# Optimization experiments

Hardware: AMD Instinct MI355X
Metric: run time of the kernel (lower is better)

## Reference

```python
import jax, jax.numpy as jnp
import numpy as np

K = 5000  # module's self.dim

def setup_inputs() -> dict:
    key = jax.random.key(0)
    x = jax.random.normal(key, (50_000_000,), dtype=jnp.float32)
    return {"x": x}

def reference(x):
    # top-k values and their indices (lax.top_k returns them sorted by value,
    # but the subsequent argsort over indices restores original-index order,
    # matching torch.topk(sorted=False) + argsort + gather exactly)
    vals, idx = jax.lax.top_k(x, K)          # [K], [K]
    order = jnp.argsort(idx)                 # permutation restoring input order
    return vals[order]                       # [K] order-preserving top-k subset
```

## Files before the change

### kernel.cpp

```cpp
#include <hip/hip_runtime.h>

#define K_TOP 5000
#define NBIN 2048
#define NB_BUCKET 4096
#define TILE4 2048
#define TARGET_SAMPLED 94u

__device__ __forceinline__ unsigned f2key(float f) {
    unsigned u = __float_as_uint(f);
    return (u & 0x80000000u) ? ~u : (u | 0x80000000u);
}
__device__ __forceinline__ float key2f(unsigned k) {
    unsigned u = (k & 0x80000000u) ? (k ^ 0x80000000u) : ~k;
    return __uint_as_float(u);
}

__global__ __launch_bounds__(256) void k_sample(const float4* __restrict__ x4, long n4,
                                                unsigned* __restrict__ hist) {
    __shared__ unsigned lh[NBIN];
    for (int i = threadIdx.x; i < NBIN; i += 256) lh[i] = 0;
    __syncthreads();
    int wave = threadIdx.x >> 6;
    int lane = threadIdx.x & 63;
    long gw = (long)blockIdx.x * 4 + wave;
    long totW = (long)gridDim.x * 4;
    long nChunk = (n4 + 8191) / 8192;
    for (long c = gw; c < nChunk; c += totW) {
        long i = c * 8192 + lane;
        if (i < n4) {
            float4 v = x4[i];
            atomicAdd(&lh[f2key(v.x) >> 21], 1u);
            atomicAdd(&lh[f2key(v.y) >> 21], 1u);
            atomicAdd(&lh[f2key(v.z) >> 21], 1u);
            atomicAdd(&lh[f2key(v.w) >> 21], 1u);
        }
    }
    __syncthreads();
    for (int i = threadIdx.x; i < NBIN; i += 256) {
        unsigned c = lh[i];
        if (c) atomicAdd(&hist[i], c);
    }
}

__global__ __launch_bounds__(256) void k_findbin(const unsigned* __restrict__ hist,
                                                 unsigned* __restrict__ ctrl) {
    __shared__ unsigned lh[NBIN];
    __shared__ unsigned gs[64];
    for (int i = threadIdx.x; i < NBIN; i += 256) lh[i] = hist[i];
    __syncthreads();
    int t = threadIdx.x;
    if (t < 64) {
        unsigned s = 0;
        for (int j = 0; j < 32; j++) s += lh[t * 32 + j];
        gs[t] = s;
    }
    __syncthreads();
    if (t == 0) {
        unsigned cum = 0;
        int g = 63;
        for (; g > 0; g--) { if (cum + gs[g] >= TARGET_SAMPLED) break; cum += gs[g]; }
        int b = g * 32 + 31;
        for (; b > g * 32; b--) { if (cum + lh[b] >= TARGET_SAMPLED) break; cum += lh[b]; }
        ctrl[1] = ((unsigned)b) << 21;
    }
}

__global__ __launch_bounds__(256) void k_compact(const float4* __restrict__ x4, long n4,
                                                 long n, const float* __restrict__ x,
                                                 unsigned* __restrict__ ctrl,
                                                 unsigned* __restrict__ candKey,
                                                 unsigned* __restrict__ candIdx,
                                                 unsigned capC) {
    unsigned L = ctrl[1];
    float Lf = key2f(L);
    long base = (long)blockIdx.x * TILE4 + threadIdx.x;
    float4 v[8];
#pragma unroll
    for (int j = 0; j < 8; j++) {
        long i = base + (long)j * 256;
        v[j] = make_float4(-1e38f, -1e38f, -1e38f, -1e38f);
        if (i < n4) v[j] = x4[i];
    }
    float m = -1e38f;
#pragma unroll
    for (int j = 0; j < 8; j++)
        m = fmaxf(m, fmaxf(fmaxf(v[j].x, v[j].y), fmaxf(v[j].z, v[j].w)));
    if (__any(m >= Lf)) {
#pragma unroll
        for (int j = 0; j < 8; j++) {
            long i = base + (long)j * 256;
            if (i < n4) {
                unsigned bb = (unsigned)(i * 4);
                const float* pv = (const float*)&v[j];
#pragma unroll
                for (int c = 0; c < 4; c++) {
                    float f = pv[c];
                    if (f >= Lf) {
                        unsigned p = atomicAdd(&ctrl[0], 1u);
                        if (p < capC) { candKey[p] = f2key(f); candIdx[p] = bb + (unsigned)c; }
                    }
                }
            }
        }
    }
    if (blockIdx.x == 0 && threadIdx.x < (int)(n & 3)) {
        float f = x[n4 * 4 + threadIdx.x];
        if (f >= Lf) {
            unsigned p = atomicAdd(&ctrl[0], 1u);
            if (p < capC) { candKey[p] = f2key(f); candIdx[p] = (unsigned)(n4 * 4 + threadIdx.x); }
        }
    }
}

__global__ __launch_bounds__(1024) void k_final(const unsigned* __restrict__ candKey,
                                                const unsigned* __restrict__ candIdx,
                                                unsigned* __restrict__ ctrl, unsigned capC,
                                                unsigned* __restrict__ selKey,
                                                unsigned* __restrict__ selIdx,
                                                unsigned* __restrict__ selKeyS,
                                                unsigned* __restrict__ selIdxS,
                                                float* __restrict__ out, long n, int bshift) {
    __shared__ unsigned h[NB_BUCKET * 2];
    __shared__ unsigned part[1024];
    __shared__ unsigned part2[32];
    __shared__ unsigned res[2];
    __shared__ unsigned sScalar;
    const int t = threadIdx.x;
    unsigned Nc = ctrl[0]; if (Nc > capC) Nc = capC;
    unsigned L = ctrl[1];

    unsigned mk = 0;
    for (unsigned i = t; i < Nc; i += 1024) { unsigned k = candKey[i]; if (k > mk) mk = k; }
    part[t] = mk;
    __syncthreads();
    if (t < 32) { unsigned m = 0; for (int j = 0; j < 32; j++) { unsigned v = part[t * 32 + j]; if (v > m) m = v; } part2[t] = m; }
    __syncthreads();
    if (t == 0) { unsigned m = 0; for (int j = 0; j < 32; j++) if (part2[j] > m) m = part2[j]; sScalar = m; }
    __syncthreads();
    unsigned maxK = sScalar;

    unsigned lo = L, target = K_TOP;
    unsigned range = maxK - lo;
    int shift = 0;
    while ((range >> shift) >= NBIN) shift++;
    for (;;) {
        int nb = (int)(range >> shift) + 1;
        for (int i = t; i < nb; i += 1024) h[i] = 0;
        __syncthreads();
        for (unsigned i = t; i < Nc; i += 1024) {
            unsigned d = candKey[i] - lo;
            if (d <= range) atomicAdd(&h[d >> shift], 1u);
        }
        __syncthreads();
        int ng = (nb + 31) >> 5;
        if (t < ng) {
            unsigned s = 0; int b0 = t * 32, e = b0 + 32; if (e > nb) e = nb;
            for (int j = b0; j < e; j++) s += h[j];
            part[t] = s;
        }
        __syncthreads();
        if (t == 0) {
            unsigned cum = 0; int g = ng - 1;
            for (; g > 0; g--) { if (cum + part[g] >= target) break; cum += part[g]; }
            int hi2 = g * 32 + 31; if (hi2 > nb - 1) hi2 = nb - 1;
            int b = hi2;
            for (; b > g * 32; b--) { if (cum + h[b] >= target) break; cum += h[b]; }
            res[0] = (unsigned)b; res[1] = target - cum;
        }
        __syncthreads();
        lo += res[0] << shift; target = res[1];
        if (shift == 0) break;
        range = (1u << shift) - 1;
        shift = (shift > 11) ? shift - 11 : 0;
    }
    unsigned T = lo, R = target;

    if (t == 0) sScalar = 0;
    __syncthreads();
    for (unsigned i = t; i < Nc; i += 1024)
        if (candKey[i] == T) atomicAdd(&sScalar, 1u);
    __syncthreads();
    unsigned cntEq = sScalar;
    unsigned idxCut = 0xFFFFFFFFu;
    if (cntEq != R) {
        unsigned lo2 = 0, tgt = R;
        unsigned range2 = (unsigned)(n - 1);
        int sh = 0;
        while ((range2 >> sh) >= NBIN) sh++;
        for (;;) {
            int nb = (int)(range2 >> sh) + 1;
            for (int i = t; i < nb; i += 1024) h[i] = 0;
            __syncthreads();
            for (unsigned i = t; i < Nc; i += 1024)
                if (candKey[i] == T) {
                    unsigned d = candIdx[i] - lo2;
                    if (d <= range2) atomicAdd(&h[d >> sh], 1u);
                }
            __syncthreads();
            int ng = (nb + 31) >> 5;
            if (t < ng) {
                unsigned s = 0; int b0 = t * 32, e = b0 + 32; if (e > nb) e = nb;
                for (int j = b0; j < e; j++) s += h[j];
                part[t] = s;
            }
            __syncthreads();
            if (t == 0) {
                unsigned cum = 0; int g = 0;
                for (; g < ng - 1; g++) { if (cum + part[g] >= tgt) break; cum += part[g]; }
                int b = g * 32; int hi2 = g * 32 + 31; if (hi2 > nb - 1) hi2 = nb - 1;
                for (; b < hi2; b++) { if (cum + h[b] >= tgt) break; cum += h[b]; }
                res[0] = (unsigned)b; res[1] = tgt - cum;
            }
            __syncthreads();
            lo2 += res[0] << sh; tgt = res[1];
            if (sh == 0) break;
            range2 = (1u << sh) - 1;
            sh = (sh > 11) ? sh - 11 : 0;
        }
        idxCut = lo2;
    }
    __syncthreads();

    for (int i = t; i < NB_BUCKET; i += 1024) h[i] = 0;
    if (t == 0) sScalar = 0;
    __syncthreads();
    for (unsigned i = t; i < Nc; i += 1024) {
        unsigned k = candKey[i]; unsigned id = candIdx[i];
        if (k > T || (k == T && id <= idxCut)) {
            unsigned p = atomicAdd(&sScalar, 1u);
            if (p < K_TOP) {
                selKey[p] = k; selIdx[p] = id;
                atomicAdd(&h[id >> bshift], 1u);
            }
        }
    }
    __syncthreads();
    unsigned nSel = sScalar; if (nSel > K_TOP) nSel = K_TOP;

    unsigned* bc = h;
    unsigned* bs = h + NB_BUCKET;
    { unsigned s = 0; for (int j = 0; j < 4; j++) s += bc[t * 4 + j]; part[t] = s; }
    __syncthreads();
    if (t < 32) { unsigned s = 0; for (int j = 0; j < 32; j++) s += part[t * 32 + j]; part2[t] = s; }
    __syncthreads();
    if (t == 0) { unsigned run = 0; for (int j = 0; j < 32; j++) { unsigned v = part2[j]; part2[j] = run; run += v; } }
    __syncthreads();
    if (t < 32) { unsigned run = part2[t]; for (int j = 0; j < 32; j++) { int id2 = t * 32 + j; unsigned v = part[id2]; part[id2] = run; run += v; } }
    __syncthreads();
    { unsigned run = part[t]; for (int j = 0; j < 4; j++) { bs[t * 4 + j] = run; run += bc[t * 4 + j]; } }
    __syncthreads();

    for (unsigned g = t; g < nSel; g += 1024) {
        unsigned id = selIdx[g];
        unsigned b = id >> bshift;
        unsigned p = atomicAdd(&bs[b], 1u);
        if (p < K_TOP) { selKeyS[p] = selKey[g]; selIdxS[p] = id; }
    }
    __syncthreads();

    for (int j = 0; j < 4; j++) {
        int b = t * 4 + j;
        unsigned cnt = bc[b];
        if (!cnt) continue;
        unsigned s = bs[b] - cnt;
        for (unsigned i = 0; i < cnt; i++) {
            unsigned mi = i, mv = selIdxS[s + i];
            for (unsigned q = i + 1; q < cnt; q++) {
                unsigned v = selIdxS[s + q];
                if (v < mv) { mv = v; mi = q; }
            }
            if (mi != i) {
                unsigned ti = selIdxS[s + i]; selIdxS[s + i] = selIdxS[s + mi]; selIdxS[s + mi] = ti;
                unsigned tk = selKeyS[s + i]; selKeyS[s + i] = selKeyS[s + mi]; selKeyS[s + mi] = tk;
            }
            out[s + i] = key2f(selKeyS[s + i]);
        }
    }
}

extern "C" void kernel_launch(void* const* d_in, const int* in_sizes, int n_in,
                              void* d_out, int out_size, void* d_ws, size_t ws_size,
                              hipStream_t stream) {
    const float* x = (const float*)d_in[0];
    long n = in_sizes[0];
    float* out = (float*)d_out;
    unsigned* w = (unsigned*)d_ws;

    unsigned* hist    = w;
    unsigned* ctrl    = w + 2048;
    unsigned* selKey  = w + 2056;
    unsigned* selIdx  = w + 7056;
    unsigned* selKeyS = w + 12056;
    unsigned* selIdxS = w + 17056;
    const size_t CAND_BASE = 24576;
    size_t words = ws_size / 4;
    unsigned capC = 0;
    if (words > CAND_BASE + 64) {
        size_t c = (words - CAND_BASE) / 2;
        if (c > (size_t)(4u << 20)) c = (size_t)(4u << 20);
        capC = (unsigned)c;
    }
    unsigned* candKey = w + CAND_BASE;
    unsigned* candIdx = candKey + capC;

    int bshift = 0;
    while (((n - 1) >> bshift) >= NB_BUCKET) bshift++;

    hipMemsetAsync(d_ws, 0, 2056u * 4u + 32u, stream);

    long n4 = n / 4;
    long nBlocks = (n4 + TILE4 - 1) / TILE4;
    k_sample<<<256, 256, 0, stream>>>((const float4*)x, n4, hist);
    k_findbin<<<1, 256, 0, stream>>>(hist, ctrl);
    k_compact<<<(int)nBlocks, 256, 0, stream>>>((const float4*)x, n4, n, x, ctrl,
                                                candKey, candIdx, capC);
    k_final<<<1, 1024, 0, stream>>>(candKey, candIdx, ctrl, capC,
                                    selKey, selIdx, selKeyS, selIdxS, out, n, bshift);
}
```

Measured before the change: 424.0 us.

## Make compact kernel grid-stride with nontemporal loads and smaller tiles

Result: slower. 444.5 us (+4.8%).

```diff
diff --git a/kernel.cpp b/kernel.cpp
--- a/kernel.cpp
+++ b/kernel.cpp
@@ -3,8 +3,9 @@
 #define K_TOP 5000
 #define NBIN 2048
 #define NB_BUCKET 4096
-#define TILE4 2048
 #define TARGET_SAMPLED 94u
+
+typedef float vfloat4 __attribute__((ext_vector_type(4)));
 
 __device__ __forceinline__ unsigned f2key(float f) {
     unsigned u = __float_as_uint(f);
@@ -65,42 +66,48 @@
     }
 }
 
-__global__ __launch_bounds__(256) void k_compact(const float4* __restrict__ x4, long n4,
-                                                 long n, const float* __restrict__ x,
-                                                 unsigned* __restrict__ ctrl,
-                                                 unsigned* __restrict__ candKey,
-                                                 unsigned* __restrict__ candIdx,
-                                                 unsigned capC) {
+__global__ __launch_bounds__(256, 8) void k_compact(const vfloat4* __restrict__ x4, long n4,
+                                                    long n, const float* __restrict__ x,
+                                                    unsigned* __restrict__ ctrl,
+                                                    unsigned* __restrict__ candKey,
+                                                    unsigned* __restrict__ candIdx,
+                                                    unsigned capC) {
     unsigned L = ctrl[1];
     float Lf = key2f(L);
-    long base = (long)blockIdx.x * TILE4 + threadIdx.x;
-    float4 v[8];
-#pragma unroll
-    for (int j = 0; j < 8; j++) {
-        long i = base + (long)j * 256;
-        v[j] = make_float4(-1e38f, -1e38f, -1e38f, -1e38f);
-        if (i < n4) v[j] = x4[i];
-    }
-    float m = -1e38f;
-#pragma unroll
-    for (int j = 0; j < 8; j++)
-        m = fmaxf(m, fmaxf(fmaxf(v[j].x, v[j].y), fmaxf(v[j].z, v[j].w)));
-    if (__any(m >= Lf)) {
-#pragma unroll
-        for (int j = 0; j < 8; j++) {
-            long i = base + (long)j * 256;
-            if (i < n4) {
-                unsigned bb = (unsigned)(i * 4);
-                const float* pv = (const float*)&v[j];
-#pragma unroll
-                for (int c = 0; c < 4; c++) {
-                    float f = pv[c];
-                    if (f >= Lf) {
-                        unsigned p = atomicAdd(&ctrl[0], 1u);
-                        if (p < capC) { candKey[p] = f2key(f); candIdx[p] = bb + (unsigned)c; }
-                    }
-                }
-            }
+    const vfloat4 neg = {-1e38f, -1e38f, -1e38f, -1e38f};
+    long tiles = (n4 + 1023) >> 10;
+    for (long tile = blockIdx.x; tile < tiles; tile += gridDim.x) {
+        long b0 = (tile << 10) + threadIdx.x;
+        long b1 = b0 + 256, b2 = b0 + 512, b3 = b0 + 768;
+        bool in0 = b0 < n4, in1 = b1 < n4, in2 = b2 < n4, in3 = b3 < n4;
+        vfloat4 v0 = neg, v1 = neg, v2 = neg, v3 = neg;
+        if (in0) v0 = __builtin_nontemporal_load(x4 + b0);
+        if (in1) v1 = __builtin_nontemporal_load(x4 + b1);
+        if (in2) v2 = __builtin_nontemporal_load(x4 + b2);
+        if (in3) v3 = __builtin_nontemporal_load(x4 + b3);
+        float m01 = fmaxf(fmaxf(fmaxf(v0.x, v0.y), fmaxf(v0.z, v0.w)),
+                          fmaxf(fmaxf(v1.x, v1.y), fmaxf(v1.z, v1.w)));
+        float m23 = fmaxf(fmaxf(fmaxf(v2.x, v2.y), fmaxf(v2.z, v2.w)),
+                          fmaxf(fmaxf(v3.x, v3.y), fmaxf(v3.z, v3.w)));
+        if (__any(fmaxf(m01, m23) >= Lf)) {
+#define PROC(vv, inb, ii)                                                        \
+            if (inb) {                                                           \
+                unsigned bb = (unsigned)((ii) * 4);                              \
+                _Pragma("unroll")                                                \
+                for (int c = 0; c < 4; c++) {                                    \
+                    float f = (vv)[c];                                           \
+                    if (f >= Lf) {                                               \
+                        unsigned p = atomicAdd(&ctrl[0], 1u);                    \
+                        if (p < capC) { candKey[p] = f2key(f);                   \
+                                        candIdx[p] = bb + (unsigned)c; }         \
+                    }                                                            \
+                }                                                                \
+            }
+            PROC(v0, in0, b0)
+            PROC(v1, in1, b1)
+            PROC(v2, in2, b2)
+            PROC(v3, in3, b3)
+#undef PROC
         }
     }
     if (blockIdx.x == 0 && threadIdx.x < (int)(n & 3)) {
@@ -306,14 +313,13 @@
     int bshift = 0;
     while (((n - 1) >> bshift) >= NB_BUCKET) bshift++;
 
-    hipMemsetAsync(d_ws, 0, 2056u * 4u + 32u, stream);
+    (void)hipMemsetAsync(d_ws, 0, 2056u * 4u + 32u, stream);
 
     long n4 = n / 4;
-    long nBlocks = (n4 + TILE4 - 1) / TILE4;
     k_sample<<<256, 256, 0, stream>>>((const float4*)x, n4, hist);
     k_findbin<<<1, 256, 0, stream>>>(hist, ctrl);
-    k_compact<<<(int)nBlocks, 256, 0, stream>>>((const float4*)x, n4, n, x, ctrl,
-                                                candKey, candIdx, capC);
+    k_compact<<<4096, 256, 0, stream>>>((const vfloat4*)x, n4, n, x, ctrl,
+                                        candKey, candIdx, capC);
     k_final<<<1, 1024, 0, stream>>>(candKey, candIdx, ctrl, capC,
                                     selKey, selIdx, selKeyS, selIdxS, out, n, bshift);
 }
```

## Rewrite compaction as grid-stride loop with four strided vector loads

Applied to the files above, without the earlier changes.

Measured after the change: 422.7 us. No clear change (-0.3%).

```diff
diff --git a/kernel.cpp b/kernel.cpp
--- a/kernel.cpp
+++ b/kernel.cpp
@@ -3,8 +3,9 @@
 #define K_TOP 5000
 #define NBIN 2048
 #define NB_BUCKET 4096
-#define TILE4 2048
 #define TARGET_SAMPLED 94u
+
+typedef float vfloat4 __attribute__((ext_vector_type(4)));
 
 __device__ __forceinline__ unsigned f2key(float f) {
     unsigned u = __float_as_uint(f);
@@ -65,51 +66,57 @@
     }
 }
 
-__global__ __launch_bounds__(256) void k_compact(const float4* __restrict__ x4, long n4,
+__global__ __launch_bounds__(256) void k_compact(const vfloat4* __restrict__ x4, long n4,
                                                  long n, const float* __restrict__ x,
                                                  unsigned* __restrict__ ctrl,
                                                  unsigned* __restrict__ candKey,
                                                  unsigned* __restrict__ candIdx,
                                                  unsigned capC) {
-    unsigned L = ctrl[1];
-    float Lf = key2f(L);
-    long base = (long)blockIdx.x * TILE4 + threadIdx.x;
-    float4 v[8];
-#pragma unroll
-    for (int j = 0; j < 8; j++) {
-        long i = base + (long)j * 256;
-        v[j] = make_float4(-1e38f, -1e38f, -1e38f, -1e38f);
-        if (i < n4) v[j] = x4[i];
-    }
-    float m = -1e38f;
-#pragma unroll
-    for (int j = 0; j < 8; j++)
-        m = fmaxf(m, fmaxf(fmaxf(v[j].x, v[j].y), fmaxf(v[j].z, v[j].w)));
-    if (__any(m >= Lf)) {
-#pragma unroll
-        for (int j = 0; j < 8; j++) {
-            long i = base + (long)j * 256;
-            if (i < n4) {
-                unsigned bb = (unsigned)(i * 4);
-                const float* pv = (const float*)&v[j];
-#pragma unroll
-                for (int c = 0; c < 4; c++) {
-                    float f = pv[c];
-                    if (f >= Lf) {
-                        unsigned p = atomicAdd(&ctrl[0], 1u);
-                        if (p < capC) { candKey[p] = f2key(f); candIdx[p] = bb + (unsigned)c; }
-                    }
-                }
-            }
-        }
-    }
-    if (blockIdx.x == 0 && threadIdx.x < (int)(n & 3)) {
-        float f = x[n4 * 4 + threadIdx.x];
-        if (f >= Lf) {
-            unsigned p = atomicAdd(&ctrl[0], 1u);
-            if (p < capC) { candKey[p] = f2key(f); candIdx[p] = (unsigned)(n4 * 4 + threadIdx.x); }
-        }
-    }
+    const float Lf = key2f(ctrl[1]);
+    const long nthreads = (long)gridDim.x * blockDim.x;
+    const long gid = (long)blockIdx.x * blockDim.x + threadIdx.x;
+    const long q = n4 >> 2;
+
+#define PUSH(f, idx)                                                     \
+    {                                                                    \
+        unsigned p = atomicAdd(&ctrl[0], 1u);                            \
+        if (p < capC) { candKey[p] = f2key(f); candIdx[p] = (idx); }     \
+    }
+#define PROC4(vv, base4)                                                 \
+    {                                                                    \
+        unsigned bb = (unsigned)((base4) * 4);                           \
+        if ((vv).x >= Lf) PUSH((vv).x, bb)                               \
+        if ((vv).y >= Lf) PUSH((vv).y, bb + 1)                           \
+        if ((vv).z >= Lf) PUSH((vv).z, bb + 2)                           \
+        if ((vv).w >= Lf) PUSH((vv).w, bb + 3)                           \
+    }
+
+    for (long i = gid; i < q; i += nthreads) {
+        vfloat4 v0 = x4[i];
+        vfloat4 v1 = x4[i + q];
+        vfloat4 v2 = x4[i + 2 * q];
+        vfloat4 v3 = x4[i + 3 * q];
+        PROC4(v0, i)
+        PROC4(v1, i + q)
+        PROC4(v2, i + 2 * q)
+        PROC4(v3, i + 3 * q)
+    }
+
+    if (blockIdx.x == 0) {
+        long rem0 = 4 * q;
+        if (threadIdx.x < (int)(n4 - rem0)) {
+            long i = rem0 + threadIdx.x;
+            vfloat4 v = x4[i];
+            PROC4(v, i)
+        }
+        int tail = (int)(n & 3);
+        if (threadIdx.x < tail) {
+            float f = x[n4 * 4 + threadIdx.x];
+            if (f >= Lf) PUSH(f, (unsigned)(n4 * 4 + threadIdx.x))
+        }
+    }
+#undef PROC4
+#undef PUSH
 }
 
 __global__ __launch_bounds__(1024) void k_final(const unsigned* __restrict__ candKey,
@@ -265,9 +272,9 @@
         unsigned s = bs[b] - cnt;
         for (unsigned i = 0; i < cnt; i++) {
             unsigned mi = i, mv = selIdxS[s + i];
-            for (unsigned q = i + 1; q < cnt; q++) {
-                unsigned v = selIdxS[s + q];
-                if (v < mv) { mv = v; mi = q; }
+            for (unsigned q2 = i + 1; q2 < cnt; q2++) {
+                unsigned v = selIdxS[s + q2];
+                if (v < mv) { mv = v; mi = q2; }
             }
             if (mi != i) {
                 unsigned ti = selIdxS[s + i]; selIdxS[s + i] = selIdxS[s + mi]; selIdxS[s + mi] = ti;
@@ -306,14 +313,13 @@
     int bshift = 0;
     while (((n - 1) >> bshift) >= NB_BUCKET) bshift++;
 
-    hipMemsetAsync(d_ws, 0, 2056u * 4u + 32u, stream);
+    (void)hipMemsetAsync(d_ws, 0, 2056u * 4u + 32u, stream);
 
     long n4 = n / 4;
-    long nBlocks = (n4 + TILE4 - 1) / TILE4;
     k_sample<<<256, 256, 0, stream>>>((const float4*)x, n4, hist);
     k_findbin<<<1, 256, 0, stream>>>(hist, ctrl);
-    k_compact<<<(int)nBlocks, 256, 0, stream>>>((const float4*)x, n4, n, x, ctrl,
-                                                candKey, candIdx, capC);
+    k_compact<<<4096, 256, 0, stream>>>((const vfloat4*)x, n4, n, x, ctrl,
+                                        candKey, candIdx, capC);
     k_final<<<1, 1024, 0, stream>>>(candKey, candIdx, ctrl, capC,
                                     selKey, selIdx, selKeyS, selIdxS, out, n, bshift);
 }
```
